# Optimization experiments

Measured on AMD Instinct MI355X. Metric: run time of the kernel, lower is better.

Reference implementation:

```python
import jax, jax.numpy as jnp
import numpy as np

HIDDEN = 2048
NUM_HEADS = 16
HEAD_DIM = HIDDEN // NUM_HEADS  # 128
LAYER_IDX = 0


def setup_inputs() -> dict:
    key = jax.random.key(0)
    k1, k2, k3, k4, k5 = jax.random.split(key, 5)
    B, S = 2, 2048
    hidden_states = jax.random.normal(k1, (B, S, HIDDEN), dtype=jnp.float32)
    # causal mask, broadcastable to attn shape (B, Q, H, K)
    causal = jnp.tril(jnp.ones((S, S), dtype=jnp.bool_))  # [Q, K]
    attention_mask = causal[None, :, None, :]  # [1, Q, 1, K]
    c_attn_w = jax.random.normal(k2, (HIDDEN, HIDDEN + 2 * HEAD_DIM), dtype=jnp.float32) * 0.02
    c_attn_b = jax.random.normal(k3, (HIDDEN + 2 * HEAD_DIM,), dtype=jnp.float32) * 0.02
    c_proj_w = jax.random.normal(k4, (HIDDEN, HIDDEN), dtype=jnp.float32) * 0.02
    c_proj_b = jax.random.normal(k5, (HIDDEN,), dtype=jnp.float32) * 0.02
    return {
        "hidden_states": hidden_states,
        "attention_mask": attention_mask,
        "c_attn_w": c_attn_w,
        "c_attn_b": c_attn_b,
        "c_proj_w": c_proj_w,
        "c_proj_b": c_proj_b,
    }


def reference(hidden_states, attention_mask, c_attn_w, c_attn_b, c_proj_w, c_proj_b):
    B, S, D = hidden_states.shape
    H, hd = NUM_HEADS, HEAD_DIM
    # c_attn then split into per-head query and shared (MQA) key/value
    qkv = hidden_states @ c_attn_w + c_attn_b  # [B, S, D + 2*hd]
    query = qkv[..., :D].reshape(B, S, H, hd)  # [B, Q, H, hd]
    k = qkv[..., D:D + hd]                     # [B, K, hd] shared across heads
    v = qkv[..., D + hd:]                      # [B, K, hd]
    # fp32 input => upcast=False => unscale=1, scale = 1/sqrt(head_dim)
    scale = 1.0 / jnp.sqrt(jnp.float32(hd))
    scores = jnp.einsum('bqhd,bkd->bqhk', query, k) * scale  # [B, Q, H, K]
    mask_value = jnp.finfo(jnp.float32).min
    scores = jnp.where(attention_mask, scores, mask_value)
    attn = jax.nn.softmax(scores, axis=-1)
    attn_output = jnp.einsum('bqhk,bkd->bqhd', attn, v).reshape(B, S, D)
    attn_output = attn_output @ c_proj_w + c_proj_b
    return attn_output
```

## Files before the change

kernel.cpp:

```cpp
#include <hip/hip_runtime.h>
#include <hip/hip_bf16.h>

typedef __bf16 bf16_t;
typedef __bf16 bf16x8 __attribute__((ext_vector_type(8)));
typedef __bf16 bf16x4 __attribute__((ext_vector_type(4)));
typedef float f32x4 __attribute__((ext_vector_type(4)));

#define S_LEN 2048
#define HID   2048
#define NH    16
#define HD    128
#define QKVN  2304
#define NEG_BIG (-30000.0f)

__device__ __forceinline__ void gld_lds16(const bf16_t* g, bf16_t* l) {
  __builtin_amdgcn_global_load_lds(
      (const __attribute__((address_space(1))) void*)((const void*)g),
      (__attribute__((address_space(3))) void*)((void*)l), 16, 0, 0);
}

__global__ __launch_bounds__(256) void cvt_f32_bf16_kernel(
    const float* __restrict__ in, bf16_t* __restrict__ out, int n)
{
  int i = (blockIdx.x * 256 + threadIdx.x) * 4;
  if (i < n) {
    float4 v = *(const float4*)(in + i);
    bf16x4 o;
    o[0] = (bf16_t)v.x; o[1] = (bf16_t)v.y; o[2] = (bf16_t)v.z; o[3] = (bf16_t)v.w;
    *(bf16x4*)(out + i) = o;
  }
}

__global__ __launch_bounds__(256) void transpose_cvt_kernel(
    const float* __restrict__ in, bf16_t* __restrict__ out, int K, int N)
{
  int nc = threadIdx.x & 63;
  int kg = threadIdx.x >> 6;
  int n  = blockIdx.x * 64 + nc;
  int kb = blockIdx.y * 32 + kg * 8;
  bf16x8 v;
  #pragma unroll
  for (int i = 0; i < 8; ++i) v[i] = (bf16_t)in[(size_t)(kb + i) * N + n];
  *(bf16x8*)(out + (size_t)n * K + kb) = v;
}

__global__ __launch_bounds__(256) void vt_extract_kernel(
    const bf16_t* __restrict__ qkv, bf16_t* __restrict__ vtg)
{
  int d  = threadIdx.x & 127;
  int sg = threadIdx.x >> 7;
  int b  = blockIdx.y;
  int s8 = blockIdx.x * 2 + sg;
  bf16x8 v;
  #pragma unroll
  for (int i = 0; i < 8; ++i)
    v[i] = qkv[((size_t)(b * S_LEN + s8 * 8 + i)) * QKVN + HID + HD + d];
  *(bf16x8*)(vtg + ((size_t)(b * HD + d)) * S_LEN + s8 * 8) = v;
}

template <typename OutT>
__global__ __launch_bounds__(256) void gemm_bias_kernel(
    const bf16_t* __restrict__ A, const bf16_t* __restrict__ WT,
    const float* __restrict__ bias, OutT* __restrict__ C,
    int K, int lda, int ldc)
{
  __shared__ bf16_t WTsh[128 * 32];

  const int tid  = threadIdx.x;
  const int wave = tid >> 6;
  const int lane = tid & 63;
  const int quad = lane >> 4;
  const int c16  = lane & 15;
  const int n0 = blockIdx.x * 128;
  const int m0 = blockIdx.y * 128;

  f32x4 acc[2][8] = {};

  bf16x8 af[2], afn[2];
  #pragma unroll
  for (int rb = 0; rb < 2; ++rb)
    af[rb] = *(const bf16x8*)(A + (size_t)(m0 + wave * 32 + rb * 16 + c16) * lda
                               + quad * 8);

  for (int k0 = 0; k0 < K; k0 += 32) {
    __syncthreads();
    #pragma unroll
    for (int j = 0; j < 2; ++j) {
      int q = (wave * 2 + j) * 64 + lane;
      int n = q >> 2, kc = q & 3;
      gld_lds16(WT + (size_t)(n0 + n) * K + k0 + kc * 8,
                WTsh + (wave * 2 + j) * 512);
    }
    __syncthreads();

    int kn = (k0 + 32 < K) ? k0 + 32 : 0;
    #pragma unroll
    for (int rb = 0; rb < 2; ++rb)
      afn[rb] = *(const bf16x8*)(A + (size_t)(m0 + wave * 32 + rb * 16 + c16) * lda
                                  + kn + quad * 8);

    #pragma unroll
    for (int nt = 0; nt < 8; ++nt) {
      bf16x8 bfrag = *(const bf16x8*)(WTsh + (c16 + nt * 16) * 32 + quad * 8);
      acc[0][nt] = __builtin_amdgcn_mfma_f32_16x16x32_bf16(af[0], bfrag, acc[0][nt], 0, 0, 0);
      acc[1][nt] = __builtin_amdgcn_mfma_f32_16x16x32_bf16(af[1], bfrag, acc[1][nt], 0, 0, 0);
    }
    af[0] = afn[0]; af[1] = afn[1];
  }

  #pragma unroll
  for (int nt = 0; nt < 8; ++nt) {
    int col = n0 + nt * 16 + c16;
    float bv = bias[col];
    #pragma unroll
    for (int rb = 0; rb < 2; ++rb) {
      int rbase = m0 + wave * 32 + rb * 16 + quad * 4;
      #pragma unroll
      for (int r = 0; r < 4; ++r)
        C[(size_t)(rbase + r) * ldc + col] = (OutT)(acc[rb][nt][r] + bv);
    }
  }
}

__global__ __launch_bounds__(512, 4) void mqa_attn_kernel(
    const bf16_t* __restrict__ qkv, const bf16_t* __restrict__ vtg,
    bf16_t* __restrict__ out)
{
  __shared__ bf16_t Ksh[2][64 * 136];
  __shared__ bf16_t VTsh[2][128 * 72];

  const int tid  = threadIdx.x;
  const int wave = tid >> 6;
  const int g    = wave >> 2;
  const int wv   = wave & 3;
  const int lane = tid & 63;
  const int quad = lane >> 4;
  const int c16  = lane & 15;
  const int gt   = tid & 255;
  const int h = blockIdx.y;
  const int b = blockIdx.z;
  const float qscale = 0.08838834764831845f * 1.4426950408889634f;

  const bf16_t* kbase = qkv + (size_t)b * S_LEN * QKVN + HID;
  const bf16_t* vtb   = vtg + (size_t)b * HD * S_LEN;

  for (int half = 0; half < 2; ++half) {
    const int qb = half ? (31 - (int)blockIdx.x) : (int)blockIdx.x;
    const int q0 = qb * 64;
    const int qrow = q0 + wv * 16 + c16;

    const bf16_t* qp = qkv + ((size_t)(b * S_LEN + qrow)) * QKVN + h * HD;
    bf16x8 qf[4];
    #pragma unroll
    for (int ks = 0; ks < 4; ++ks) {
      bf16x8 t = *(const bf16x8*)(qp + ks * 32 + quad * 8);
      #pragma unroll
      for (int j = 0; j < 8; ++j) t[j] = (bf16_t)((float)t[j] * qscale);
      qf[ks] = t;
    }

    float m_q = NEG_BIG, l_q = 0.0f;
    f32x4 o[8] = {};
    const int nss = (qb + 2) >> 1;

    for (int ss = 0; ss < nss; ++ss) {
      const int kt = 2 * ss + g;
      const bool active = (kt <= qb);

      __syncthreads();
      if (active) {
        for (int c = gt; c < 1024; c += 256) {
          int key = c >> 4, dc = c & 15;
          *(bf16x8*)(&Ksh[g][key * 136 + dc * 8]) =
              *(const bf16x8*)(kbase + (size_t)(kt * 64 + key) * QKVN + dc * 8);
        }
        for (int c = gt; c < 1024; c += 256) {
          int d = c >> 3, kc = c & 7;
          *(bf16x8*)(&VTsh[g][d * 72 + kc * 8]) =
              *(const bf16x8*)(vtb + (size_t)d * S_LEN + kt * 64 + kc * 8);
        }
      }
      __syncthreads();

      float p[4][4];
      if (active) {
        f32x4 sacc[4] = {};
        #pragma unroll
        for (int mt = 0; mt < 4; ++mt) {
          #pragma unroll
          for (int ks = 0; ks < 4; ++ks) {
            bf16x8 kf = *(const bf16x8*)(&Ksh[g][(mt * 16 + c16) * 136 + ks * 32 + quad * 8]);
            sacc[mt] = __builtin_amdgcn_mfma_f32_16x16x32_bf16(kf, qf[ks], sacc[mt], 0, 0, 0);
          }
        }
        float mx = NEG_BIG;
        if (kt == qb) {
          #pragma unroll
          for (int mt = 0; mt < 4; ++mt) {
            #pragma unroll
            for (int r = 0; r < 4; ++r) {
              int key = kt * 64 + mt * 16 + quad * 4 + r;
              float v = sacc[mt][r];
              if (key > qrow) v = NEG_BIG;
              p[mt][r] = v;
              mx = fmaxf(mx, v);
            }
          }
        } else {
          #pragma unroll
          for (int mt = 0; mt < 4; ++mt) {
            #pragma unroll
            for (int r = 0; r < 4; ++r) {
              p[mt][r] = sacc[mt][r];
              mx = fmaxf(mx, sacc[mt][r]);
            }
          }
        }
        mx = fmaxf(mx, __shfl_xor(mx, 16));
        mx = fmaxf(mx, __shfl_xor(mx, 32));

        float mn = fmaxf(m_q, mx);
        float alpha = __builtin_exp2f(m_q - mn);
        m_q = mn;

        float rs = 0.f;
        #pragma unroll
        for (int mt = 0; mt < 4; ++mt) {
          #pragma unroll
          for (int r = 0; r < 4; ++r) {
            float pe = __builtin_exp2f(p[mt][r] - m_q);
            p[mt][r] = pe;
            rs += pe;
          }
        }
        rs += __shfl_xor(rs, 16);
        rs += __shfl_xor(rs, 32);
        l_q = l_q * alpha + rs;
        #pragma unroll
        for (int mt8 = 0; mt8 < 8; ++mt8) {
          #pragma unroll
          for (int r = 0; r < 4; ++r) o[mt8][r] *= alpha;
        }
      }

      __syncthreads();
      if (active) {
        bf16_t* Pw = &Ksh[g][(wv * 16) * 136];
        #pragma unroll
        for (int mt = 0; mt < 4; ++mt) {
          bf16x4 pk;
          #pragma unroll
          for (int r = 0; r < 4; ++r) pk[r] = (bf16_t)p[mt][r];
          *(bf16x4*)(Pw + c16 * 136 + mt * 16 + quad * 4) = pk;
        }
        bf16x8 pf[2];
        #pragma unroll
        for (int kh = 0; kh < 2; ++kh)
          pf[kh] = *(const bf16x8*)(Pw + c16 * 136 + kh * 32 + quad * 8);
        #pragma unroll
        for (int mt8 = 0; mt8 < 8; ++mt8) {
          #pragma unroll
          for (int kh = 0; kh < 2; ++kh) {
            bf16x8 vf = *(const bf16x8*)(&VTsh[g][(mt8 * 16 + c16) * 72 + kh * 32 + quad * 8]);
            o[mt8] = __builtin_amdgcn_mfma_f32_16x16x32_bf16(vf, pf[kh], o[mt8], 0, 0, 0);
          }
        }
      }
    }

    __syncthreads();
    float* scr = (float*)&VTsh[0][0];
    float* mls = scr + 4 * 16 * 132;
    if (g == 1) {
      float* op = scr + (wv * 16 + c16) * 132;
      #pragma unroll
      for (int mt8 = 0; mt8 < 8; ++mt8)
        *(f32x4*)(op + mt8 * 16 + quad * 4) = o[mt8];
      if (quad == 0) {
        mls[wv * 32 + c16] = m_q;
        mls[wv * 32 + 16 + c16] = l_q;
      }
    }
    __syncthreads();
    if (g == 0) {
      float m1 = mls[wv * 32 + c16];
      float l1 = mls[wv * 32 + 16 + c16];
      float mF = fmaxf(m_q, m1);
      float a0 = __builtin_exp2f(m_q - mF);
      float a1 = __builtin_exp2f(m1 - mF);
      float inv = 1.0f / fmaxf(a0 * l_q + a1 * l1, 1e-20f);
      a0 *= inv; a1 *= inv;
      const float* op = scr + (wv * 16 + c16) * 132;
      bf16_t* Osh = &Ksh[0][(wv * 16) * 136];
      #pragma unroll
      for (int mt8 = 0; mt8 < 8; ++mt8) {
        f32x4 o1 = *(const f32x4*)(op + mt8 * 16 + quad * 4);
        bf16x4 pk;
        #pragma unroll
        for (int r = 0; r < 4; ++r) pk[r] = (bf16_t)(o[mt8][r] * a0 + o1[r] * a1);
        *(bf16x4*)(Osh + c16 * 136 + mt8 * 16 + quad * 4) = pk;
      }
      int ql = lane >> 2, dc = lane & 3;
      #pragma unroll
      for (int i = 0; i < 4; ++i) {
        bf16x8 v = *(const bf16x8*)(Osh + ql * 136 + dc * 8 + i * 32);
        *(bf16x8*)(out + ((size_t)(b * S_LEN + q0 + wv * 16 + ql)) * HID
                       + h * HD + dc * 8 + i * 32) = v;
      }
    }
  }
}

extern "C" void kernel_launch(void* const* d_in, const int* in_sizes, int n_in,
                              void* d_out, int out_size, void* d_ws, size_t ws_size,
                              hipStream_t stream) {
  const float* hidden_f   = (const float*)d_in[0];
  const float* c_attn_w_f = (const float*)d_in[2];
  const float* c_attn_b_f = (const float*)d_in[3];
  const float* c_proj_w_f = (const float*)d_in[4];
  const float* c_proj_b_f = (const float*)d_in[5];
  float* out = (float*)d_out;

  const int M = 2 * S_LEN;
  const int nH  = M * HID;
  const int nWq = HID * QKVN;
  const int nWp = HID * HID;

  bf16_t* hbf   = (bf16_t*)d_ws;
  bf16_t* wqT   = hbf  + nH;
  bf16_t* wpT   = wqT  + nWq;
  bf16_t* qkv   = wpT  + nWp;
  bf16_t* attn  = qkv  + (size_t)M * QKVN;
  bf16_t* vtg   = attn + (size_t)M * HID;

  cvt_f32_bf16_kernel<<<nH / 1024, 256, 0, stream>>>(hidden_f, hbf, nH);
  dim3 gt1(QKVN / 64, HID / 32);
  transpose_cvt_kernel<<<gt1, 256, 0, stream>>>(c_attn_w_f, wqT, HID, QKVN);
  dim3 gt2(HID / 64, HID / 32);
  transpose_cvt_kernel<<<gt2, 256, 0, stream>>>(c_proj_w_f, wpT, HID, HID);

  dim3 g1(QKVN / 128, M / 128);
  gemm_bias_kernel<bf16_t><<<g1, 256, 0, stream>>>(hbf, wqT, c_attn_b_f, qkv,
                                                   HID, HID, QKVN);

  dim3 gv(S_LEN / 16, 2);
  vt_extract_kernel<<<gv, 256, 0, stream>>>(qkv, vtg);

  dim3 g2(16, NH, 2);
  mqa_attn_kernel<<<g2, 512, 0, stream>>>(qkv, vtg, attn);

  dim3 g3(HID / 128, M / 128);
  gemm_bias_kernel<float><<<g3, 256, 0, stream>>>(attn, wpT, c_proj_b_f, out,
                                                  HID, HID, HID);
}
```

Before: 352.3 us.

## Stage A tiles in LDS and use 2x2 wave tiling in GEMM

The GEMM now loads both the A and WT k-slices into shared memory with global_load_lds and splits work across waves as a 2x2 grid of 64x64 subtiles, each holding 4x4 MFMA accumulators. Before, each wave read its A fragments straight from global memory into registers, prefetched one step ahead, and covered all 128 columns. The new layout balances A and B fragment reuse per wave and swaps scattered global A reads for coalesced LDS staging. In exchange it drops the register prefetch of A, so global loads are no longer overlapped with MFMA, and the 32-element LDS row stride may cause bank conflicts.

```diff
diff --git a/kernel.cpp b/kernel.cpp
--- a/kernel.cpp
+++ b/kernel.cpp
@@ -64,57 +64,56 @@
     const float* __restrict__ bias, OutT* __restrict__ C,
     int K, int lda, int ldc)
 {
-  __shared__ bf16_t WTsh[128 * 32];
+  __shared__ bf16_t Ash[128 * 32];
+  __shared__ bf16_t Bsh[128 * 32];
 
   const int tid  = threadIdx.x;
   const int wave = tid >> 6;
   const int lane = tid & 63;
   const int quad = lane >> 4;
   const int c16  = lane & 15;
+  const int wm = wave >> 1;
+  const int wn = wave & 1;
   const int n0 = blockIdx.x * 128;
   const int m0 = blockIdx.y * 128;
 
-  f32x4 acc[2][8] = {};
-
-  bf16x8 af[2], afn[2];
-  #pragma unroll
-  for (int rb = 0; rb < 2; ++rb)
-    af[rb] = *(const bf16x8*)(A + (size_t)(m0 + wave * 32 + rb * 16 + c16) * lda
-                               + quad * 8);
+  f32x4 acc[4][4] = {};
 
   for (int k0 = 0; k0 < K; k0 += 32) {
     __syncthreads();
     #pragma unroll
     for (int j = 0; j < 2; ++j) {
-      int q = (wave * 2 + j) * 64 + lane;
-      int n = q >> 2, kc = q & 3;
-      gld_lds16(WT + (size_t)(n0 + n) * K + k0 + kc * 8,
-                WTsh + (wave * 2 + j) * 512);
+      int cbase = wave * 128 + j * 64;
+      int c = cbase + lane;
+      int row = c >> 2, kc = c & 3;
+      gld_lds16(A  + (size_t)(m0 + row) * lda + k0 + kc * 8, Ash + cbase * 8);
+      gld_lds16(WT + (size_t)(n0 + row) * K   + k0 + kc * 8, Bsh + cbase * 8);
     }
     __syncthreads();
 
-    int kn = (k0 + 32 < K) ? k0 + 32 : 0;
-    #pragma unroll
-    for (int rb = 0; rb < 2; ++rb)
-      afn[rb] = *(const bf16x8*)(A + (size_t)(m0 + wave * 32 + rb * 16 + c16) * lda
-                                  + kn + quad * 8);
-
-    #pragma unroll
-    for (int nt = 0; nt < 8; ++nt) {
-      bf16x8 bfrag = *(const bf16x8*)(WTsh + (c16 + nt * 16) * 32 + quad * 8);
-      acc[0][nt] = __builtin_amdgcn_mfma_f32_16x16x32_bf16(af[0], bfrag, acc[0][nt], 0, 0, 0);
-      acc[1][nt] = __builtin_amdgcn_mfma_f32_16x16x32_bf16(af[1], bfrag, acc[1][nt], 0, 0, 0);
-    }
-    af[0] = afn[0]; af[1] = afn[1];
+    bf16x8 af[4], bfr[4];
+    #pragma unroll
+    for (int rb = 0; rb < 4; ++rb)
+      af[rb] = *(const bf16x8*)(Ash + (wm * 64 + rb * 16 + c16) * 32 + quad * 8);
+    #pragma unroll
+    for (int nt = 0; nt < 4; ++nt)
+      bfr[nt] = *(const bf16x8*)(Bsh + (wn * 64 + nt * 16 + c16) * 32 + quad * 8);
+
+    #pragma unroll
+    for (int rb = 0; rb < 4; ++rb)
+      #pragma unroll
+      for (int nt = 0; nt < 4; ++nt)
+        acc[rb][nt] = __builtin_amdgcn_mfma_f32_16x16x32_bf16(af[rb], bfr[nt],
+                                                              acc[rb][nt], 0, 0, 0);
   }
 
   #pragma unroll
-  for (int nt = 0; nt < 8; ++nt) {
-    int col = n0 + nt * 16 + c16;
+  for (int nt = 0; nt < 4; ++nt) {
+    int col = n0 + wn * 64 + nt * 16 + c16;
     float bv = bias[col];
     #pragma unroll
-    for (int rb = 0; rb < 2; ++rb) {
-      int rbase = m0 + wave * 32 + rb * 16 + quad * 4;
+    for (int rb = 0; rb < 4; ++rb) {
+      int rbase = m0 + wm * 64 + rb * 16 + quad * 4;
       #pragma unroll
       for (int r = 0; r < 4; ++r)
         C[(size_t)(rbase + r) * ldc + col] = (OutT)(acc[rb][nt][r] + bv);
```

Result: faster. 343.5 us (-2.5%).
